# Kernel tuning notes

Hardware: AMD Instinct MI355X
Metric: run time of the kernel (lower is better)

The kernel has to match this reference:

```python
import jax, jax.numpy as jnp
import numpy as np

D_MODEL = 1024
N_HEADS = 16
D_HEAD = D_MODEL // N_HEADS
WINDOW = 256
ATTN_SCALE = 1.0
SCALE = float(np.sqrt(D_HEAD))
NEG = -10000.0


def setup_inputs() -> dict:
    key = jax.random.key(0)
    ks = jax.random.split(key, 7)
    B, S = 2, 2048
    q = jax.random.normal(ks[0], (B, S, D_MODEL), dtype=jnp.float32)
    k = jax.random.normal(ks[1], (B, S, D_MODEL), dtype=jnp.float32)
    v = jax.random.normal(ks[2], (B, S, D_MODEL), dtype=jnp.float32)
    # Xavier-uniform-like scale for square linear weights: sqrt(6/(fan_in+fan_out))
    lim = float(np.sqrt(6.0 / (D_MODEL + D_MODEL)))
    def xavier(kk):
        return jax.random.uniform(kk, (D_MODEL, D_MODEL), minval=-lim, maxval=lim, dtype=jnp.float32)
    return {"q": q, "k": k, "v": v,
            "WQ": xavier(ks[3]), "WK": xavier(ks[4]),
            "WV": xavier(ks[5]), "WO": xavier(ks[6])}


def _split_heads(x):
    B, S, _ = x.shape
    return x.reshape(B, S, N_HEADS, D_HEAD).transpose(0, 2, 1, 3)  # [B,H,S,Dh]


def reference(q, k, v, WQ, WK, WV, WO):
    B, Sq, _ = q.shape
    Sk = k.shape[1]
    # torch nn.Linear: y = x @ W.T
    qh = _split_heads(q @ WQ.T) / SCALE          # [B,H,Sq,Dh]
    kh = _split_heads(k @ WK.T)                  # [B,H,Sk,Dh]
    vh = _split_heads(v @ WV.T)                  # [B,H,Sk,Dh]
    scores = jnp.einsum('bhqd,bhkd->bhqk', qh, kh) * ATTN_SCALE
    # global abs-max normalization (clamped at 1)
    scores = scores / jnp.maximum(jnp.max(jnp.abs(scores)), 1.0)
    # sliding window mask: key j visible to query i iff i-WINDOW+1 <= j <= i
    qi = jnp.arange(Sq)[:, None]
    kj = jnp.arange(Sk)[None, :]
    win = (kj <= qi) & (kj > qi - WINDOW)        # [Sq,Sk] bool
    scores = jnp.where(win[None, None], scores, NEG)
    attn = jax.nn.softmax(scores, axis=-1)
    out = jnp.einsum('bhqk,bhkd->bhqd', attn, vh)
    out = out.transpose(0, 2, 1, 3).reshape(B, Sq, D_MODEL)
    out = out @ WO.T
    out = out / jnp.maximum(jnp.mean(jnp.abs(out)), 1.0)
    return out
```

## Files before the change

### kernel.cpp

```cpp
#include <hip/hip_runtime.h>
#include <hip/hip_bf16.h>

#define S_LEN 2048
#define DM    1024
#define NH    16
#define DH    64
#define WIN   256
#define BATCH 2

using f32x4   = __attribute__((ext_vector_type(4))) float;
using bf16x8  = __attribute__((ext_vector_type(8))) short;
using ushort8 = __attribute__((ext_vector_type(8))) unsigned short;

static __device__ __forceinline__ unsigned short f2bf(float f) {
  unsigned int x = __float_as_uint(f);
  x += 0x7fffu + ((x >> 16) & 1u);
  return (unsigned short)(x >> 16);
}

typedef const __attribute__((address_space(1))) void* gas_t;
typedef __attribute__((address_space(3))) void* las_t;
static __device__ __forceinline__ void gload16(const void* g, void* l) {
  __builtin_amdgcn_global_load_lds((gas_t)g, (las_t)l, 16, 0, 0);
}

__global__ void k_init(unsigned int* absmax) { *absmax = 0u; }

__global__ __launch_bounds__(256) void k_cvt_all(const float* __restrict__ w0,
                                                 const float* __restrict__ w1,
                                                 const float* __restrict__ w2,
                                                 const float* __restrict__ w3,
                                                 const float* __restrict__ q,
                                                 const float* __restrict__ k,
                                                 const float* __restrict__ v,
                                                 unsigned short* __restrict__ Wb,
                                                 unsigned short* __restrict__ qb,
                                                 unsigned short* __restrict__ kb,
                                                 unsigned short* __restrict__ vb) {
  const int z = blockIdx.z;
  const float* src;
  unsigned short* dst;
  int n8;
  if (z < 4) {
    src = (z == 0) ? w0 : (z == 1) ? w1 : (z == 2) ? w2 : w3;
    dst = Wb + (size_t)z * DM * DM;
    n8 = (DM * DM) / 8;
  } else {
    src = (z == 4) ? q : (z == 5) ? k : v;
    dst = (z == 4) ? qb : (z == 5) ? kb : vb;
    n8 = (BATCH * S_LEN * DM) / 8;
  }
  int i = blockIdx.x * blockDim.x + threadIdx.x;
  int stride = gridDim.x * blockDim.x;
  for (; i < n8; i += stride) {
    float4 f0 = ((const float4*)src)[2 * i];
    float4 f1 = ((const float4*)src)[2 * i + 1];
    ushort8 u;
    u[0] = f2bf(f0.x); u[1] = f2bf(f0.y); u[2] = f2bf(f0.z); u[3] = f2bf(f0.w);
    u[4] = f2bf(f1.x); u[5] = f2bf(f1.y); u[6] = f2bf(f1.z); u[7] = f2bf(f1.w);
    ((ushort8*)dst)[i] = u;
  }
}

__device__ __forceinline__ void gemm128_core(const unsigned short* __restrict__ A,
                                             const unsigned short* __restrict__ Bw,
                                             void* __restrict__ Cptr, float oscale,
                                             int omode, bool swap, int R0, int C0) {
  __shared__ unsigned short As[2][128][64];
  __shared__ unsigned short Bs[2][128][64];
  const int tid = threadIdx.x, lane = tid & 63, w = tid >> 6;
  const int wr = w >> 1, wc = w & 1;

  int srow[4], scol[4];
#pragma unroll
  for (int c = 0; c < 4; ++c) {
    srow[c] = c * 32 + w * 8 + (lane >> 3);
    scol[c] = ((lane & 7) ^ (srow[c] & 7)) << 3;
  }

  f32x4 z = {0.f, 0.f, 0.f, 0.f};
  f32x4 acc[4][4];
#pragma unroll
  for (int i = 0; i < 4; ++i)
#pragma unroll
    for (int j = 0; j < 4; ++j) acc[i][j] = z;

  unsigned short* Af0 = &As[0][0][0];
  unsigned short* Bf0 = &Bs[0][0][0];
  const int cb = 16 * (lane >> 4);

#define STAGE_G(buf, k0) do {                                                          \
    unsigned short* Ad = Af0 + (buf) * 8192 + w * 512;                                 \
    unsigned short* Bd = Bf0 + (buf) * 8192 + w * 512;                                 \
    _Pragma("unroll")                                                                  \
    for (int c = 0; c < 4; ++c) {                                                      \
      gload16(A  + (size_t)(R0 + srow[c]) * DM + (k0) + scol[c], Ad + c * 2048);       \
      gload16(Bw + (size_t)(C0 + srow[c]) * DM + (k0) + scol[c], Bd + c * 2048);       \
    }                                                                                  \
  } while (0)

  STAGE_G(0, 0);
  __syncthreads();

  for (int t = 0; t < 16; ++t) {
    const int cur = t & 1;
    if (t + 1 < 16) STAGE_G(cur ^ 1, (t + 1) * 64);

    const char* Af = (const char*)(Af0 + cur * 8192);
    const char* Bf = (const char*)(Bf0 + cur * 8192);
    bf16x8 av[4][2], bv[4][2];
#pragma unroll
    for (int i = 0; i < 4; ++i) {
      int row = 64 * wr + 16 * i + (lane & 15);
      int sw = (row & 7) << 4;
      const char* rp = Af + row * 128;
      av[i][0] = *(const bf16x8*)(rp + (cb ^ sw));
      av[i][1] = *(const bf16x8*)(rp + ((cb + 64) ^ sw));
    }
#pragma unroll
    for (int j = 0; j < 4; ++j) {
      int row = 64 * wc + 16 * j + (lane & 15);
      int sw = (row & 7) << 4;
      const char* rp = Bf + row * 128;
      bv[j][0] = *(const bf16x8*)(rp + (cb ^ sw));
      bv[j][1] = *(const bf16x8*)(rp + ((cb + 64) ^ sw));
    }
    if (swap) {
#pragma unroll
      for (int i = 0; i < 4; ++i)
#pragma unroll
        for (int j = 0; j < 4; ++j) {
          acc[i][j] = __builtin_amdgcn_mfma_f32_16x16x32_bf16(bv[j][0], av[i][0], acc[i][j], 0, 0, 0);
          acc[i][j] = __builtin_amdgcn_mfma_f32_16x16x32_bf16(bv[j][1], av[i][1], acc[i][j], 0, 0, 0);
        }
    } else {
#pragma unroll
      for (int i = 0; i < 4; ++i)
#pragma unroll
        for (int j = 0; j < 4; ++j) {
          acc[i][j] = __builtin_amdgcn_mfma_f32_16x16x32_bf16(av[i][0], bv[j][0], acc[i][j], 0, 0, 0);
          acc[i][j] = __builtin_amdgcn_mfma_f32_16x16x32_bf16(av[i][1], bv[j][1], acc[i][j], 0, 0, 0);
        }
    }
    __syncthreads();
  }
#undef STAGE_G

#pragma unroll
  for (int i = 0; i < 4; ++i) {
#pragma unroll
    for (int j = 0; j < 4; ++j) {
      if (swap) {
        int grow  = R0 + 64 * wr + 16 * i + (lane & 15);
        int gcol0 = C0 + 64 * wc + 16 * j + 4 * (lane >> 4);
        if (omode == 0) {
          float4 st = {acc[i][j][0] * oscale, acc[i][j][1] * oscale,
                       acc[i][j][2] * oscale, acc[i][j][3] * oscale};
          *(float4*)((float*)Cptr + (size_t)grow * DM + gcol0) = st;
        } else {
          int b = grow >> 11, s = grow & (S_LEN - 1);
          int h = gcol0 >> 6, d0 = gcol0 & 63;
          ushort4 st = {f2bf(acc[i][j][0] * oscale), f2bf(acc[i][j][1] * oscale),
                        f2bf(acc[i][j][2] * oscale), f2bf(acc[i][j][3] * oscale)};
          *(ushort4*)((unsigned short*)Cptr + (((size_t)(b * NH + h) * S_LEN + s) << 6) + d0) = st;
        }
      } else {
        int grow0 = R0 + 64 * wr + 16 * i + 4 * (lane >> 4);
        int gcol  = C0 + 64 * wc + 16 * j + (lane & 15);
        int b = grow0 >> 11, s0 = grow0 & (S_LEN - 1);
        int h = gcol >> 6, d = gcol & 63;
        ushort4 st = {f2bf(acc[i][j][0] * oscale), f2bf(acc[i][j][1] * oscale),
                      f2bf(acc[i][j][2] * oscale), f2bf(acc[i][j][3] * oscale)};
        *(ushort4*)((unsigned short*)Cptr + (((size_t)(b * NH + h) * DH + d) << 11) + s0) = st;
      }
    }
  }
}

__global__ __launch_bounds__(256) void k_gemm_qkv(const unsigned short* __restrict__ qb,
                                                  const unsigned short* __restrict__ kb,
                                                  const unsigned short* __restrict__ vb,
                                                  const unsigned short* __restrict__ WbQ,
                                                  const unsigned short* __restrict__ WbK,
                                                  const unsigned short* __restrict__ WbV,
                                                  unsigned short* __restrict__ qh,
                                                  unsigned short* __restrict__ kh,
                                                  unsigned short* __restrict__ vt) {
  const unsigned short *A, *B;
  unsigned short* C;
  float sc;
  int om;
  bool sw;
  if (blockIdx.z == 0)      { A = qb; B = WbQ; C = qh; sc = 0.125f; om = 1; sw = true;  }
  else if (blockIdx.z == 1) { A = kb; B = WbK; C = kh; sc = 1.0f;   om = 1; sw = true;  }
  else                      { A = vb; B = WbV; C = vt; sc = 1.0f;   om = 2; sw = false; }
  gemm128_core(A, B, C, sc, om, sw, blockIdx.x * 128, blockIdx.y * 128);
}

__global__ __launch_bounds__(256) void k_gemm_out(const unsigned short* __restrict__ A,
                                                  const unsigned short* __restrict__ Bw,
                                                  float* __restrict__ C) {
  gemm128_core(A, Bw, C, 1.0f, 0, true, blockIdx.x * 128, blockIdx.y * 128);
}

__global__ __launch_bounds__(256) void k_scoresmax(const unsigned short* __restrict__ qh,
                                                   const unsigned short* __restrict__ kh,
                                                   unsigned int* __restrict__ absmax) {
  __shared__ unsigned short Ks[2][128][64];
  const int tid = threadIdx.x, lane = tid & 63, w = tid >> 6;
  const size_t base = (size_t)blockIdx.y * S_LEN * DH;
  const unsigned short* Q = qh + base;
  const unsigned short* K = kh + base;
  const int q0 = blockIdx.x * 128;

  bf16x8 a[2][2];
#pragma unroll
  for (int rb = 0; rb < 2; ++rb) {
    const unsigned short* qr = Q + (size_t)(q0 + 32 * w + 16 * rb + (lane & 15)) * DH + 8 * (lane >> 4);
    a[rb][0] = *(const bf16x8*)qr;
    a[rb][1] = *(const bf16x8*)(qr + 32);
  }

  int srow[4], scol[4];
#pragma unroll
  for (int c = 0; c < 4; ++c) {
    srow[c] = c * 32 + w * 8 + (lane >> 3);
    scol[c] = ((lane & 7) ^ (srow[c] & 7)) << 3;
  }
  unsigned short* Kf0 = &Ks[0][0][0];
  const int cbb = 16 * (lane >> 4);

#define STAGE_K(buf, kc) do {                                                          \
    unsigned short* Kd = Kf0 + (buf) * 8192 + w * 512;                                 \
    _Pragma("unroll")                                                                  \
    for (int c = 0; c < 4; ++c)                                                        \
      gload16(K + (size_t)((kc) + srow[c]) * DH + scol[c], Kd + c * 2048);             \
  } while (0)

  STAGE_K(0, 0);
  __syncthreads();

  float m = 0.f;
  for (int t = 0; t < 16; ++t) {
    const int cur = t & 1;
    if (t + 1 < 16) STAGE_K(cur ^ 1, (t + 1) * 128);
    const char* Kf = (const char*)(Kf0 + cur * 8192);
#pragma unroll
    for (int cb = 0; cb < 8; ++cb) {
      int row = 16 * cb + (lane & 15);
      int sw = (row & 7) << 4;
      const char* rp = Kf + row * 128;
      bf16x8 b0 = *(const bf16x8*)(rp + (cbb ^ sw));
      bf16x8 b1 = *(const bf16x8*)(rp + ((cbb + 64) ^ sw));
#pragma unroll
      for (int rb = 0; rb < 2; ++rb) {
        f32x4 acc = {0.f, 0.f, 0.f, 0.f};
        acc = __builtin_amdgcn_mfma_f32_16x16x32_bf16(a[rb][0], b0, acc, 0, 0, 0);
        acc = __builtin_amdgcn_mfma_f32_16x16x32_bf16(a[rb][1], b1, acc, 0, 0, 0);
        m = fmaxf(m, fmaxf(fmaxf(fabsf(acc[0]), fabsf(acc[1])), fmaxf(fabsf(acc[2]), fabsf(acc[3]))));
      }
    }
    __syncthreads();
  }
#undef STAGE_K

#pragma unroll
  for (int mk = 1; mk < 64; mk <<= 1) m = fmaxf(m, __shfl_xor(m, mk, 64));
  __shared__ float red[4];
  if (lane == 0) red[w] = m;
  __syncthreads();
  if (threadIdx.x == 0)
    atomicMax(absmax, __float_as_uint(fmaxf(fmaxf(red[0], red[1]), fmaxf(red[2], red[3]))));
}

#define NT 10
__global__ __launch_bounds__(256) void k_attn(const unsigned short* __restrict__ qh,
                                              const unsigned short* __restrict__ kh,
                                              const unsigned short* __restrict__ vt,
                                              const unsigned int* __restrict__ absmax,
                                              unsigned short* __restrict__ attn_c) {
  __shared__ unsigned short Ks[2][32][72];
  __shared__ unsigned short Vts[2][64][40];
  __shared__ unsigned short Pl[4][16][40];
  const int tid = threadIdx.x, lane = tid & 63, w = tid >> 6;
  const int bh = blockIdx.y, b = bh >> 4, h = bh & 15;
  const int Q0 = blockIdx.x * 64;
  const int kstart = Q0 - WIN;
  const size_t base = (size_t)bh * S_LEN * DH;
  const unsigned short* Kb = kh + base;
  const unsigned short* Vtb = vt + base;

  const int skrow = tid >> 3, skcol = (tid & 7) << 3;
  const int svd = tid >> 2, svcol = (tid & 3) << 3;

  const float invM = 1.0f / fmaxf(__uint_as_float(*absmax), 1.0f);
  const unsigned short* Qp = qh + base + (size_t)(Q0 + 16 * w + (lane & 15)) * DH + 8 * (lane >> 4);
  bf16x8 a0 = *(const bf16x8*)Qp;
  bf16x8 a1 = *(const bf16x8*)(Qp + 32);

  ushort8 rk, rv;
  ushort8 zz = {0, 0, 0, 0, 0, 0, 0, 0};
#define LOADT(T) do {                                                        \
    int kk = kstart + 32 * (T) + skrow;                                      \
    rk = (kk >= 0) ? *(const ushort8*)(Kb + (size_t)kk * DH + skcol) : zz;   \
    int kc = kstart + 32 * (T) + svcol;                                      \
    rv = (kc >= 0) ? *(const ushort8*)(Vtb + (size_t)svd * S_LEN + kc) : zz; \
  } while (0)
#define WRITET(buf) do {                                                     \
    *(ushort8*)&Ks[buf][skrow][skcol] = rk;                                  \
    *(ushort8*)&Vts[buf][svd][svcol] = rv;                                   \
  } while (0)

  LOADT(0);
  WRITET(0);
  __syncthreads();

  const int Tlo = w >> 1, Thi = (w >> 1) + 8;
  const int qrow = Q0 + 16 * w + 4 * (lane >> 4);
  float sm[4] = {0.f, 0.f, 0.f, 0.f};
  f32x4 z = {0.f, 0.f, 0.f, 0.f};
  f32x4 o[4];
#pragma unroll
  for (int i = 0; i < 4; ++i) o[i] = z;

  for (int T = 0; T < NT; ++T) {
    const int cur = T & 1;
    const bool act = (T >= Tlo) && (T <= Thi);
    if (T + 1 < NT) LOADT(T + 1);
    if (act) {
      f32x4 p[2];
#pragma unroll
      for (int cb = 0; cb < 2; ++cb) {
        const unsigned short* kr = &Ks[cur][16 * cb + (lane & 15)][8 * (lane >> 4)];
        bf16x8 b0 = *(const bf16x8*)kr;
        bf16x8 b1 = *(const bf16x8*)(kr + 32);
        f32x4 a = z;
        a = __builtin_amdgcn_mfma_f32_16x16x32_bf16(a0, b0, a, 0, 0, 0);
        a = __builtin_amdgcn_mfma_f32_16x16x32_bf16(a1, b1, a, 0, 0, 0);
        p[cb] = a;
      }
#pragma unroll
      for (int cb = 0; cb < 2; ++cb) {
        int kcol = kstart + 32 * T + 16 * cb + (lane & 15);
#pragma unroll
        for (int r = 0; r < 4; ++r) {
          int qq = qrow + r;
          bool ok = (kcol >= 0) && (kcol <= qq) && (kcol + WIN > qq);
          float e = ok ? __expf(p[cb][r] * invM) : 0.f;
          sm[r] += e;
          Pl[w][4 * (lane >> 4) + r][16 * cb + (lane & 15)] = f2bf(e);
        }
      }
    }
    __syncthreads();
    if (act) {
      bf16x8 pa = *(const bf16x8*)&Pl[w][lane & 15][8 * (lane >> 4)];
#pragma unroll
      for (int dt = 0; dt < 4; ++dt) {
        bf16x8 bv = *(const bf16x8*)&Vts[cur][16 * dt + (lane & 15)][8 * (lane >> 4)];
        o[dt] = __builtin_amdgcn_mfma_f32_16x16x32_bf16(pa, bv, o[dt], 0, 0, 0);
      }
    }
    if (T + 1 < NT) WRITET((T + 1) & 1);
    __syncthreads();
  }

#pragma unroll
  for (int r = 0; r < 4; ++r) {
#pragma unroll
    for (int mk = 1; mk < 16; mk <<= 1) sm[r] += __shfl_xor(sm[r], mk, 64);
    sm[r] = 1.0f / sm[r];
  }
#pragma unroll
  for (int dt = 0; dt < 4; ++dt) {
#pragma unroll
    for (int r = 0; r < 4; ++r) {
      int qq = qrow + r;
      float val = o[dt][r] * sm[r];
      attn_c[((size_t)(b * S_LEN + qq) << 10) + h * DH + 16 * dt + (lane & 15)] = f2bf(val);
    }
  }
#undef LOADT
#undef WRITET
}

__global__ __launch_bounds__(256) void k_abspart(const float* __restrict__ x,
                                                 float* __restrict__ part, int n4) {
  float s = 0.f;
  for (int i = blockIdx.x * blockDim.x + threadIdx.x; i < n4; i += gridDim.x * blockDim.x) {
    float4 f = ((const float4*)x)[i];
    s += fabsf(f.x) + fabsf(f.y) + fabsf(f.z) + fabsf(f.w);
  }
#pragma unroll
  for (int mk = 1; mk < 64; mk <<= 1) s += __shfl_xor(s, mk, 64);
  __shared__ float red[4];
  if ((threadIdx.x & 63) == 0) red[threadIdx.x >> 6] = s;
  __syncthreads();
  if (threadIdx.x == 0) part[blockIdx.x] = red[0] + red[1] + red[2] + red[3];
}

__global__ __launch_bounds__(256) void k_absfinal(const float* __restrict__ part,
                                                  float* __restrict__ denominv,
                                                  int n, float invcnt) {
  float s = 0.f;
  for (int i = threadIdx.x; i < n; i += 256) s += part[i];
#pragma unroll
  for (int mk = 1; mk < 64; mk <<= 1) s += __shfl_xor(s, mk, 64);
  __shared__ float red[4];
  if ((threadIdx.x & 63) == 0) red[threadIdx.x >> 6] = s;
  __syncthreads();
  if (threadIdx.x == 0) denominv[0] = 1.0f / fmaxf(s * invcnt, 1.0f);
}

__global__ __launch_bounds__(256) void k_scale(float* __restrict__ x,
                                               const float* __restrict__ denominv, int n4) {
  float d = denominv[0];
  for (int i = blockIdx.x * blockDim.x + threadIdx.x; i < n4; i += gridDim.x * blockDim.x) {
    float4 f = ((float4*)x)[i];
    f.x *= d; f.y *= d; f.z *= d; f.w *= d;
    ((float4*)x)[i] = f;
  }
}

extern "C" void kernel_launch(void* const* d_in, const int* in_sizes, int n_in,
                              void* d_out, int out_size, void* d_ws, size_t ws_size,
                              hipStream_t stream) {
  (void)in_sizes; (void)n_in; (void)out_size; (void)ws_size;
  const float* q  = (const float*)d_in[0];
  const float* k  = (const float*)d_in[1];
  const float* v  = (const float*)d_in[2];
  const float* WQ = (const float*)d_in[3];
  const float* WK = (const float*)d_in[4];
  const float* WV = (const float*)d_in[5];
  const float* WO = (const float*)d_in[6];

  const size_t HS = (size_t)BATCH * NH * S_LEN * DH;
  unsigned short* qb     = (unsigned short*)d_ws;
  unsigned short* kb     = qb + HS;
  unsigned short* vb     = kb + HS;
  unsigned short* qh     = vb + HS;
  unsigned short* kh     = qh + HS;
  unsigned short* vt     = kh + HS;
  unsigned short* Wb     = vt + HS;
  char* scal             = (char*)(Wb + 4 * (size_t)DM * DM);
  unsigned int* absmax   = (unsigned int*)scal;
  float* denominv        = (float*)(scal + 4);
  float* partials        = (float*)(scal + 16);
  unsigned short* attn_c = qb;

  unsigned short* WbQ = Wb;
  unsigned short* WbK = Wb + (size_t)DM * DM;
  unsigned short* WbV = Wb + 2 * (size_t)DM * DM;
  unsigned short* WbO = Wb + 3 * (size_t)DM * DM;

  k_init<<<1, 1, 0, stream>>>(absmax);
  k_cvt_all<<<dim3(128, 1, 7), 256, 0, stream>>>(WQ, WK, WV, WO, q, k, v, Wb, qb, kb, vb);

  k_gemm_qkv<<<dim3(32, 8, 3), 256, 0, stream>>>(qb, kb, vb, WbQ, WbK, WbV, qh, kh, vt);

  k_scoresmax<<<dim3(16, 32), 256, 0, stream>>>(qh, kh, absmax);
  k_attn<<<dim3(32, 32), 256, 0, stream>>>(qh, kh, vt, absmax, attn_c);

  k_gemm_out<<<dim3(32, 8), 256, 0, stream>>>(attn_c, WbO, (float*)d_out);

  k_abspart<<<1024, 256, 0, stream>>>((const float*)d_out, partials, (int)(HS / 4));
  k_absfinal<<<1, 256, 0, stream>>>(partials, denominv, 1024, 1.0f / (float)HS);
  k_scale<<<1024, 256, 0, stream>>>((float*)d_out, denominv, (int)(HS / 4));
}
```

Before: 147.1 us.

## Fuse abs-sum into output GEMM, shrink K tile, merge init and finalize kernels

The output GEMM epilogue now computes per-block abs-sum partials, which removes the separate abs-reduction pass over the output. The absfinal and scale kernels are merged, with each block reducing the 256 partials itself, and the absmax init is folded into the conversion kernel. This cuts three launches and one full read of the output. Separately, the GEMM K-tile drops from 64 to 32 with a new swizzle, halving LDS use per block at the cost of twice as many barrier-synchronised iterations.

After: 154.5 us. 5.1% more time.

```diff
diff --git a/kernel.cpp b/kernel.cpp
--- a/kernel.cpp
+++ b/kernel.cpp
@@ -23,8 +23,6 @@
 static __device__ __forceinline__ void gload16(const void* g, void* l) {
   __builtin_amdgcn_global_load_lds((gas_t)g, (las_t)l, 16, 0, 0);
 }
-
-__global__ void k_init(unsigned int* absmax) { *absmax = 0u; }
 
 __global__ __launch_bounds__(256) void k_cvt_all(const float* __restrict__ w0,
                                                  const float* __restrict__ w1,
@@ -36,8 +34,10 @@
                                                  unsigned short* __restrict__ Wb,
                                                  unsigned short* __restrict__ qb,
                                                  unsigned short* __restrict__ kb,
-                                                 unsigned short* __restrict__ vb) {
+                                                 unsigned short* __restrict__ vb,
+                                                 unsigned int* __restrict__ absmax) {
   const int z = blockIdx.z;
+  if (z == 0 && blockIdx.x == 0 && threadIdx.x == 0) *absmax = 0u;
   const float* src;
   unsigned short* dst;
   int n8;
@@ -65,18 +65,17 @@
 __device__ __forceinline__ void gemm128_core(const unsigned short* __restrict__ A,
                                              const unsigned short* __restrict__ Bw,
                                              void* __restrict__ Cptr, float oscale,
-                                             int omode, bool swap, int R0, int C0) {
-  __shared__ unsigned short As[2][128][64];
-  __shared__ unsigned short Bs[2][128][64];
+                                             int omode, bool swap, int R0, int C0,
+                                             float* __restrict__ partials, int pbid) {
+  __shared__ unsigned short As[2][128][32];
+  __shared__ unsigned short Bs[2][128][32];
+  __shared__ float red[4];
   const int tid = threadIdx.x, lane = tid & 63, w = tid >> 6;
   const int wr = w >> 1, wc = w & 1;
 
-  int srow[4], scol[4];
-#pragma unroll
-  for (int c = 0; c < 4; ++c) {
-    srow[c] = c * 32 + w * 8 + (lane >> 3);
-    scol[c] = ((lane & 7) ^ (srow[c] & 7)) << 3;
-  }
+  const int s_row = w * 16 + (lane >> 2);
+  const int s_col = ((lane & 3) ^ ((lane >> 3) & 3)) << 3;
+  const int rbyte = (((lane >> 4) ^ ((lane >> 1) & 3)) << 4);
 
   f32x4 z = {0.f, 0.f, 0.f, 0.f};
   f32x4 acc[4][4];
@@ -87,65 +86,49 @@
 
   unsigned short* Af0 = &As[0][0][0];
   unsigned short* Bf0 = &Bs[0][0][0];
-  const int cb = 16 * (lane >> 4);
-
-#define STAGE_G(buf, k0) do {                                                          \
-    unsigned short* Ad = Af0 + (buf) * 8192 + w * 512;                                 \
-    unsigned short* Bd = Bf0 + (buf) * 8192 + w * 512;                                 \
-    _Pragma("unroll")                                                                  \
-    for (int c = 0; c < 4; ++c) {                                                      \
-      gload16(A  + (size_t)(R0 + srow[c]) * DM + (k0) + scol[c], Ad + c * 2048);       \
-      gload16(Bw + (size_t)(C0 + srow[c]) * DM + (k0) + scol[c], Bd + c * 2048);       \
-    }                                                                                  \
+
+#define STAGE_G(buf, k0) do {                                                      \
+    unsigned short* Ad = Af0 + (buf) * 4096 + w * 512;                             \
+    unsigned short* Bd = Bf0 + (buf) * 4096 + w * 512;                             \
+    gload16(A  + (size_t)(R0 + s_row) * DM + (k0) + s_col, Ad);                    \
+    gload16(A  + (size_t)(R0 + 64 + s_row) * DM + (k0) + s_col, Ad + 2048);        \
+    gload16(Bw + (size_t)(C0 + s_row) * DM + (k0) + s_col, Bd);                    \
+    gload16(Bw + (size_t)(C0 + 64 + s_row) * DM + (k0) + s_col, Bd + 2048);        \
   } while (0)
 
   STAGE_G(0, 0);
   __syncthreads();
 
-  for (int t = 0; t < 16; ++t) {
+  for (int t = 0; t < 32; ++t) {
     const int cur = t & 1;
-    if (t + 1 < 16) STAGE_G(cur ^ 1, (t + 1) * 64);
-
-    const char* Af = (const char*)(Af0 + cur * 8192);
-    const char* Bf = (const char*)(Bf0 + cur * 8192);
-    bf16x8 av[4][2], bv[4][2];
+    if (t + 1 < 32) STAGE_G(cur ^ 1, (t + 1) * 32);
+
+    const char* Af = (const char*)(Af0 + cur * 4096);
+    const char* Bf = (const char*)(Bf0 + cur * 4096);
+    bf16x8 av[4], bv[4];
 #pragma unroll
     for (int i = 0; i < 4; ++i) {
-      int row = 64 * wr + 16 * i + (lane & 15);
-      int sw = (row & 7) << 4;
-      const char* rp = Af + row * 128;
-      av[i][0] = *(const bf16x8*)(rp + (cb ^ sw));
-      av[i][1] = *(const bf16x8*)(rp + ((cb + 64) ^ sw));
-    }
-#pragma unroll
-    for (int j = 0; j < 4; ++j) {
-      int row = 64 * wc + 16 * j + (lane & 15);
-      int sw = (row & 7) << 4;
-      const char* rp = Bf + row * 128;
-      bv[j][0] = *(const bf16x8*)(rp + (cb ^ sw));
-      bv[j][1] = *(const bf16x8*)(rp + ((cb + 64) ^ sw));
+      av[i] = *(const bf16x8*)(Af + (64 * wr + 16 * i + (lane & 15)) * 64 + rbyte);
+      bv[i] = *(const bf16x8*)(Bf + (64 * wc + 16 * i + (lane & 15)) * 64 + rbyte);
     }
     if (swap) {
 #pragma unroll
       for (int i = 0; i < 4; ++i)
 #pragma unroll
-        for (int j = 0; j < 4; ++j) {
-          acc[i][j] = __builtin_amdgcn_mfma_f32_16x16x32_bf16(bv[j][0], av[i][0], acc[i][j], 0, 0, 0);
-          acc[i][j] = __builtin_amdgcn_mfma_f32_16x16x32_bf16(bv[j][1], av[i][1], acc[i][j], 0, 0, 0);
-        }
+        for (int j = 0; j < 4; ++j)
+          acc[i][j] = __builtin_amdgcn_mfma_f32_16x16x32_bf16(bv[j], av[i], acc[i][j], 0, 0, 0);
     } else {
 #pragma unroll
       for (int i = 0; i < 4; ++i)
 #pragma unroll
-        for (int j = 0; j < 4; ++j) {
-          acc[i][j] = __builtin_amdgcn_mfma_f32_16x16x32_bf16(av[i][0], bv[j][0], acc[i][j], 0, 0, 0);
-          acc[i][j] = __builtin_amdgcn_mfma_f32_16x16x32_bf16(av[i][1], bv[j][1], acc[i][j], 0, 0, 0);
-        }
+        for (int j = 0; j < 4; ++j)
+          acc[i][j] = __builtin_amdgcn_mfma_f32_16x16x32_bf16(av[i], bv[j], acc[i][j], 0, 0, 0);
     }
     __syncthreads();
   }
 #undef STAGE_G
 
+  float s = 0.f;
 #pragma unroll
   for (int i = 0; i < 4; ++i) {
 #pragma unroll
@@ -156,13 +139,14 @@
         if (omode == 0) {
           float4 st = {acc[i][j][0] * oscale, acc[i][j][1] * oscale,
                        acc[i][j][2] * oscale, acc[i][j][3] * oscale};
+          s += fabsf(st.x) + fabsf(st.y) + fabsf(st.z) + fabsf(st.w);
           *(float4*)((float*)Cptr + (size_t)grow * DM + gcol0) = st;
         } else {
-          int b = grow >> 11, s = grow & (S_LEN - 1);
+          int b = grow >> 11, ss = grow & (S_LEN - 1);
           int h = gcol0 >> 6, d0 = gcol0 & 63;
           ushort4 st = {f2bf(acc[i][j][0] * oscale), f2bf(acc[i][j][1] * oscale),
                         f2bf(acc[i][j][2] * oscale), f2bf(acc[i][j][3] * oscale)};
-          *(ushort4*)((unsigned short*)Cptr + (((size_t)(b * NH + h) * S_LEN + s) << 6) + d0) = st;
+          *(ushort4*)((unsigned short*)Cptr + (((size_t)(b * NH + h) * S_LEN + ss) << 6) + d0) = st;
         }
       } else {
         int grow0 = R0 + 64 * wr + 16 * i + 4 * (lane >> 4);
@@ -174,6 +158,13 @@
         *(ushort4*)((unsigned short*)Cptr + (((size_t)(b * NH + h) * DH + d) << 11) + s0) = st;
       }
     }
+  }
+  if (partials) {
+#pragma unroll
+    for (int mk = 1; mk < 64; mk <<= 1) s += __shfl_xor(s, mk, 64);
+    if (lane == 0) red[w] = s;
+    __syncthreads();
+    if (tid == 0) partials[pbid] = red[0] + red[1] + red[2] + red[3];
   }
 }
 
@@ -194,13 +185,15 @@
   if (blockIdx.z == 0)      { A = qb; B = WbQ; C = qh; sc = 0.125f; om = 1; sw = true;  }
   else if (blockIdx.z == 1) { A = kb; B = WbK; C = kh; sc = 1.0f;   om = 1; sw = true;  }
   else                      { A = vb; B = WbV; C = vt; sc = 1.0f;   om = 2; sw = false; }
-  gemm128_core(A, B, C, sc, om, sw, blockIdx.x * 128, blockIdx.y * 128);
+  gemm128_core(A, B, C, sc, om, sw, blockIdx.x * 128, blockIdx.y * 128, nullptr, 0);
 }
 
 __global__ __launch_bounds__(256) void k_gemm_out(const unsigned short* __restrict__ A,
                                                   const unsigned short* __restrict__ Bw,
-                                                  float* __restrict__ C) {
-  gemm128_core(A, Bw, C, 1.0f, 0, true, blockIdx.x * 128, blockIdx.y * 128);
+                                                  float* __restrict__ C,
+                                                  float* __restrict__ partials) {
+  gemm128_core(A, Bw, C, 1.0f, 0, true, blockIdx.x * 128, blockIdx.y * 128,
+               partials, blockIdx.x + gridDim.x * blockIdx.y);
 }
 
 __global__ __launch_bounds__(256) void k_scoresmax(const unsigned short* __restrict__ qh,
@@ -384,37 +377,16 @@
 #undef WRITET
 }
 
-__global__ __launch_bounds__(256) void k_abspart(const float* __restrict__ x,
-                                                 float* __restrict__ part, int n4) {
-  float s = 0.f;
-  for (int i = blockIdx.x * blockDim.x + threadIdx.x; i < n4; i += gridDim.x * blockDim.x) {
-    float4 f = ((const float4*)x)[i];
-    s += fabsf(f.x) + fabsf(f.y) + fabsf(f.z) + fabsf(f.w);
-  }
+__global__ __launch_bounds__(256) void k_scale_final(float* __restrict__ x,
+                                                     const float* __restrict__ partials,
+                                                     float invcnt, int n4) {
+  __shared__ float red[4];
+  float s = partials[threadIdx.x];
 #pragma unroll
   for (int mk = 1; mk < 64; mk <<= 1) s += __shfl_xor(s, mk, 64);
-  __shared__ float red[4];
   if ((threadIdx.x & 63) == 0) red[threadIdx.x >> 6] = s;
   __syncthreads();
-  if (threadIdx.x == 0) part[blockIdx.x] = red[0] + red[1] + red[2] + red[3];
-}
-
-__global__ __launch_bounds__(256) void k_absfinal(const float* __restrict__ part,
-                                                  float* __restrict__ denominv,
-                                                  int n, float invcnt) {
-  float s = 0.f;
-  for (int i = threadIdx.x; i < n; i += 256) s += part[i];
-#pragma unroll
-  for (int mk = 1; mk < 64; mk <<= 1) s += __shfl_xor(s, mk, 64);
-  __shared__ float red[4];
-  if ((threadIdx.x & 63) == 0) red[threadIdx.x >> 6] = s;
-  __syncthreads();
-  if (threadIdx.x == 0) denominv[0] = 1.0f / fmaxf(s * invcnt, 1.0f);
-}
-
-__global__ __launch_bounds__(256) void k_scale(float* __restrict__ x,
-                                               const float* __restrict__ denominv, int n4) {
-  float d = denominv[0];
+  float d = 1.0f / fmaxf((red[0] + red[1] + red[2] + red[3]) * invcnt, 1.0f);
   for (int i = blockIdx.x * blockDim.x + threadIdx.x; i < n4; i += gridDim.x * blockDim.x) {
     float4 f = ((float4*)x)[i];
     f.x *= d; f.y *= d; f.z *= d; f.w *= d;
@@ -444,7 +416,6 @@
   unsigned short* Wb     = vt + HS;
   char* scal             = (char*)(Wb + 4 * (size_t)DM * DM);
   unsigned int* absmax   = (unsigned int*)scal;
-  float* denominv        = (float*)(scal + 4);
   float* partials        = (float*)(scal + 16);
   unsigned short* attn_c = qb;
 
@@ -453,17 +424,14 @@
   unsigned short* WbV = Wb + 2 * (size_t)DM * DM;
   unsigned short* WbO = Wb + 3 * (size_t)DM * DM;
 
-  k_init<<<1, 1, 0, stream>>>(absmax);
-  k_cvt_all<<<dim3(128, 1, 7), 256, 0, stream>>>(WQ, WK, WV, WO, q, k, v, Wb, qb, kb, vb);
+  k_cvt_all<<<dim3(128, 1, 7), 256, 0, stream>>>(WQ, WK, WV, WO, q, k, v, Wb, qb, kb, vb, absmax);
 
   k_gemm_qkv<<<dim3(32, 8, 3), 256, 0, stream>>>(qb, kb, vb, WbQ, WbK, WbV, qh, kh, vt);
 
   k_scoresmax<<<dim3(16, 32), 256, 0, stream>>>(qh, kh, absmax);
   k_attn<<<dim3(32, 32), 256, 0, stream>>>(qh, kh, vt, absmax, attn_c);
 
-  k_gemm_out<<<dim3(32, 8), 256, 0, stream>>>(attn_c, WbO, (float*)d_out);
-
-  k_abspart<<<1024, 256, 0, stream>>>((const float*)d_out, partials, (int)(HS / 4));
-  k_absfinal<<<1, 256, 0, stream>>>(partials, denominv, 1024, 1.0f / (float)HS);
-  k_scale<<<1024, 256, 0, stream>>>((float*)d_out, denominv, (int)(HS / 4));
-}
+  k_gemm_out<<<dim3(32, 8), 256, 0, stream>>>(attn_c, WbO, (float*)d_out, partials);
+
+  k_scale_final<<<1024, 256, 0, stream>>>((float*)d_out, partials, 1.0f / (float)HS, (int)(HS / 4));
+}
```

## Fuse abs-sum reduction into output GEMM epilogue and drop extra launches

Applied to the files above, without the earlier changes.

The output GEMM epilogue now accumulates per-block sums of absolute values and writes one partial per block (256 partials). A single scale kernel reduces the 256 partials in every block and applies the normalization, replacing the separate abspart, absfinal and scale kernels. The absmax init is folded into the conversion kernel, removing a tiny launch. This saves one full read pass over the 16 MB output and two launches, at the cost of every scale block redundantly reducing 256 partials.

Result: faster. 138.0 us (-6.2%).

```diff
diff --git a/kernel.cpp b/kernel.cpp
--- a/kernel.cpp
+++ b/kernel.cpp
@@ -23,8 +23,6 @@
 static __device__ __forceinline__ void gload16(const void* g, void* l) {
   __builtin_amdgcn_global_load_lds((gas_t)g, (las_t)l, 16, 0, 0);
 }
-
-__global__ void k_init(unsigned int* absmax) { *absmax = 0u; }
 
 __global__ __launch_bounds__(256) void k_cvt_all(const float* __restrict__ w0,
                                                  const float* __restrict__ w1,
@@ -36,8 +34,10 @@
                                                  unsigned short* __restrict__ Wb,
                                                  unsigned short* __restrict__ qb,
                                                  unsigned short* __restrict__ kb,
-                                                 unsigned short* __restrict__ vb) {
+                                                 unsigned short* __restrict__ vb,
+                                                 unsigned int* __restrict__ absmax) {
   const int z = blockIdx.z;
+  if (z == 0 && blockIdx.x == 0 && threadIdx.x == 0) *absmax = 0u;
   const float* src;
   unsigned short* dst;
   int n8;
@@ -65,9 +65,11 @@
 __device__ __forceinline__ void gemm128_core(const unsigned short* __restrict__ A,
                                              const unsigned short* __restrict__ Bw,
                                              void* __restrict__ Cptr, float oscale,
-                                             int omode, bool swap, int R0, int C0) {
+                                             int omode, bool swap, int R0, int C0,
+                                             float* __restrict__ partials, int pbid) {
   __shared__ unsigned short As[2][128][64];
   __shared__ unsigned short Bs[2][128][64];
+  __shared__ float red[4];
   const int tid = threadIdx.x, lane = tid & 63, w = tid >> 6;
   const int wr = w >> 1, wc = w & 1;
 
@@ -146,6 +148,7 @@
   }
 #undef STAGE_G
 
+  float s = 0.f;
 #pragma unroll
   for (int i = 0; i < 4; ++i) {
 #pragma unroll
@@ -156,13 +159,14 @@
         if (omode == 0) {
           float4 st = {acc[i][j][0] * oscale, acc[i][j][1] * oscale,
                        acc[i][j][2] * oscale, acc[i][j][3] * oscale};
+          s += fabsf(st.x) + fabsf(st.y) + fabsf(st.z) + fabsf(st.w);
           *(float4*)((float*)Cptr + (size_t)grow * DM + gcol0) = st;
         } else {
-          int b = grow >> 11, s = grow & (S_LEN - 1);
+          int b = grow >> 11, ss = grow & (S_LEN - 1);
           int h = gcol0 >> 6, d0 = gcol0 & 63;
           ushort4 st = {f2bf(acc[i][j][0] * oscale), f2bf(acc[i][j][1] * oscale),
                         f2bf(acc[i][j][2] * oscale), f2bf(acc[i][j][3] * oscale)};
-          *(ushort4*)((unsigned short*)Cptr + (((size_t)(b * NH + h) * S_LEN + s) << 6) + d0) = st;
+          *(ushort4*)((unsigned short*)Cptr + (((size_t)(b * NH + h) * S_LEN + ss) << 6) + d0) = st;
         }
       } else {
         int grow0 = R0 + 64 * wr + 16 * i + 4 * (lane >> 4);
@@ -174,6 +178,13 @@
         *(ushort4*)((unsigned short*)Cptr + (((size_t)(b * NH + h) * DH + d) << 11) + s0) = st;
       }
     }
+  }
+  if (partials) {
+#pragma unroll
+    for (int mk = 1; mk < 64; mk <<= 1) s += __shfl_xor(s, mk, 64);
+    if (lane == 0) red[w] = s;
+    __syncthreads();
+    if (tid == 0) partials[pbid] = red[0] + red[1] + red[2] + red[3];
   }
 }
 
@@ -194,13 +205,15 @@
   if (blockIdx.z == 0)      { A = qb; B = WbQ; C = qh; sc = 0.125f; om = 1; sw = true;  }
   else if (blockIdx.z == 1) { A = kb; B = WbK; C = kh; sc = 1.0f;   om = 1; sw = true;  }
   else                      { A = vb; B = WbV; C = vt; sc = 1.0f;   om = 2; sw = false; }
-  gemm128_core(A, B, C, sc, om, sw, blockIdx.x * 128, blockIdx.y * 128);
+  gemm128_core(A, B, C, sc, om, sw, blockIdx.x * 128, blockIdx.y * 128, nullptr, 0);
 }
 
 __global__ __launch_bounds__(256) void k_gemm_out(const unsigned short* __restrict__ A,
                                                   const unsigned short* __restrict__ Bw,
-                                                  float* __restrict__ C) {
-  gemm128_core(A, Bw, C, 1.0f, 0, true, blockIdx.x * 128, blockIdx.y * 128);
+                                                  float* __restrict__ C,
+                                                  float* __restrict__ partials) {
+  gemm128_core(A, Bw, C, 1.0f, 0, true, blockIdx.x * 128, blockIdx.y * 128,
+               partials, blockIdx.x + gridDim.x * blockIdx.y);
 }
 
 __global__ __launch_bounds__(256) void k_scoresmax(const unsigned short* __restrict__ qh,
@@ -384,37 +397,16 @@
 #undef WRITET
 }
 
-__global__ __launch_bounds__(256) void k_abspart(const float* __restrict__ x,
-                                                 float* __restrict__ part, int n4) {
-  float s = 0.f;
-  for (int i = blockIdx.x * blockDim.x + threadIdx.x; i < n4; i += gridDim.x * blockDim.x) {
-    float4 f = ((const float4*)x)[i];
-    s += fabsf(f.x) + fabsf(f.y) + fabsf(f.z) + fabsf(f.w);
-  }
+__global__ __launch_bounds__(256) void k_scale_final(float* __restrict__ x,
+                                                     const float* __restrict__ partials,
+                                                     float invcnt, int n4) {
+  __shared__ float red[4];
+  float s = partials[threadIdx.x];
 #pragma unroll
   for (int mk = 1; mk < 64; mk <<= 1) s += __shfl_xor(s, mk, 64);
-  __shared__ float red[4];
   if ((threadIdx.x & 63) == 0) red[threadIdx.x >> 6] = s;
   __syncthreads();
-  if (threadIdx.x == 0) part[blockIdx.x] = red[0] + red[1] + red[2] + red[3];
-}
-
-__global__ __launch_bounds__(256) void k_absfinal(const float* __restrict__ part,
-                                                  float* __restrict__ denominv,
-                                                  int n, float invcnt) {
-  float s = 0.f;
-  for (int i = threadIdx.x; i < n; i += 256) s += part[i];
-#pragma unroll
-  for (int mk = 1; mk < 64; mk <<= 1) s += __shfl_xor(s, mk, 64);
-  __shared__ float red[4];
-  if ((threadIdx.x & 63) == 0) red[threadIdx.x >> 6] = s;
-  __syncthreads();
-  if (threadIdx.x == 0) denominv[0] = 1.0f / fmaxf(s * invcnt, 1.0f);
-}
-
-__global__ __launch_bounds__(256) void k_scale(float* __restrict__ x,
-                                               const float* __restrict__ denominv, int n4) {
-  float d = denominv[0];
+  float d = 1.0f / fmaxf((red[0] + red[1] + red[2] + red[3]) * invcnt, 1.0f);
   for (int i = blockIdx.x * blockDim.x + threadIdx.x; i < n4; i += gridDim.x * blockDim.x) {
     float4 f = ((float4*)x)[i];
     f.x *= d; f.y *= d; f.z *= d; f.w *= d;
@@ -444,7 +436,6 @@
   unsigned short* Wb     = vt + HS;
   char* scal             = (char*)(Wb + 4 * (size_t)DM * DM);
   unsigned int* absmax   = (unsigned int*)scal;
-  float* denominv        = (float*)(scal + 4);
   float* partials        = (float*)(scal + 16);
   unsigned short* attn_c = qb;
 
@@ -453,17 +444,14 @@
   unsigned short* WbV = Wb + 2 * (size_t)DM * DM;
   unsigned short* WbO = Wb + 3 * (size_t)DM * DM;
 
-  k_init<<<1, 1, 0, stream>>>(absmax);
-  k_cvt_all<<<dim3(128, 1, 7), 256, 0, stream>>>(WQ, WK, WV, WO, q, k, v, Wb, qb, kb, vb);
+  k_cvt_all<<<dim3(128, 1, 7), 256, 0, stream>>>(WQ, WK, WV, WO, q, k, v, Wb, qb, kb, vb, absmax);
 
   k_gemm_qkv<<<dim3(32, 8, 3), 256, 0, stream>>>(qb, kb, vb, WbQ, WbK, WbV, qh, kh, vt);
 
   k_scoresmax<<<dim3(16, 32), 256, 0, stream>>>(qh, kh, absmax);
   k_attn<<<dim3(32, 32), 256, 0, stream>>>(qh, kh, vt, absmax, attn_c);
 
-  k_gemm_out<<<dim3(32, 8), 256, 0, stream>>>(attn_c, WbO, (float*)d_out);
-
-  k_abspart<<<1024, 256, 0, stream>>>((const float*)d_out, partials, (int)(HS / 4));
-  k_absfinal<<<1, 256, 0, stream>>>(partials, denominv, 1024, 1.0f / (float)HS);
-  k_scale<<<1024, 256, 0, stream>>>((float*)d_out, denominv, (int)(HS / 4));
-}
+  k_gemm_out<<<dim3(32, 8), 256, 0, stream>>>(attn_c, WbO, (float*)d_out, partials);
+
+  k_scale_final<<<1024, 256, 0, stream>>>((float*)d_out, partials, 1.0f / (float)HS, (int)(HS / 4));
+}
```
